# Optimization experiments

Hardware: AMD Instinct MI355X
Metric: run time of the kernel (lower is better)

## Reference

```python
import jax, jax.numpy as jnp
import numpy as np

NUM_HEADS = 12
SEG_HEADS = 6  # first 6 heads -> full attention; rest -> 4-way strided
HEAD_DIM = 64


def setup_inputs() -> dict:
    key = jax.random.key(0)
    ks = jax.random.split(key, 7)
    B, S, H = 2, 4096, 768
    sc = 0.02
    return {
        "hidden_states": jax.random.normal(ks[0], (B, S, H), jnp.float32),
        "Wq": jax.random.normal(ks[1], (H, H), jnp.float32) * sc,
        "bq": jax.random.normal(ks[2], (H,), jnp.float32) * sc,
        "Wk": jax.random.normal(ks[3], (H, H), jnp.float32) * sc,
        "bk": jax.random.normal(ks[4], (H,), jnp.float32) * sc,
        "Wv": jax.random.normal(ks[5], (H, H), jnp.float32) * sc,
        "bv": jax.random.normal(ks[6], (H,), jnp.float32) * sc,
    }


def _heads(x, B, S):
    # [B,S,H] -> [B,nH,S,D]
    return x.reshape(B, S, NUM_HEADS, HEAD_DIM).transpose(0, 2, 1, 3)


def reference(hidden_states, Wq, bq, Wk, bk, Wv, bv):
    B, S, H = hidden_states.shape
    scale = 1.0 / jnp.sqrt(jnp.float32(HEAD_DIM))

    q = _heads(hidden_states @ Wq.T + bq, B, S)
    k = _heads(hidden_states @ Wk.T + bk, B, S)
    v = _heads(hidden_states @ Wv.T + bv, B, S)

    # ---- full attention on first SEG_HEADS heads ----
    qf, kf, vf = q[:, :SEG_HEADS], k[:, :SEG_HEADS], v[:, :SEG_HEADS]
    scores = jnp.einsum('bhqd,bhkd->bhqk', qf, kf) * scale
    z_full = jnp.einsum('bhqk,bhkd->bhqd', jax.nn.softmax(scores, axis=-1), vf)

    # ---- 4-way strided attention on remaining heads ----
    # x[:,:,i::4,:] == reshape(B,h,S//4,4,D)[..., i, :]; batch the 4 groups.
    S4 = S // 4
    def strided(x):
        # [B,h,S,D] -> [B,h,4,S//4,D], group g holds positions g::4
        return x[:, SEG_HEADS:].reshape(B, NUM_HEADS - SEG_HEADS, S4, 4, HEAD_DIM).transpose(0, 1, 3, 2, 4)
    qa, ka, va = strided(q), strided(k), strided(v)
    s_ax = jnp.einsum('bhgqd,bhgkd->bhgqk', qa, ka) * scale
    z_ax = jnp.einsum('bhgqk,bhgkd->bhgqd', jax.nn.softmax(s_ax, axis=-1), va)
    # re-interleave: torch.stack(dim=3).view -> position s*4+g from (g,s)
    z_axis = z_ax.transpose(0, 1, 3, 2, 4).reshape(B, NUM_HEADS - SEG_HEADS, S, HEAD_DIM)

    ctx = jnp.concatenate([z_full, z_axis], axis=1)           # [B,nH,S,D]
    ctx = ctx.transpose(0, 2, 1, 3).reshape(B, S, NUM_HEADS * HEAD_DIM)
    return ctx
```

## Files before the change

### kernel.cpp

```cpp
#include <hip/hip_runtime.h>
#include <stdint.h>
#include <math.h>

#define BB 2
#define SS 4096
#define NHEADS 12
#define DHEAD 64

#define N_HS (8192*768)
#define N_W  (768*768)

typedef __bf16 bf16x8 __attribute__((ext_vector_type(8)));
typedef float  f32x4  __attribute__((ext_vector_type(4)));
typedef float  f32x16 __attribute__((ext_vector_type(16)));

__device__ __forceinline__ unsigned short f2bf(float x) {
  union { float f; uint32_t u; } v; v.f = x;
  uint32_t r = v.u + 0x7fffu + ((v.u >> 16) & 1u);
  return (unsigned short)(r >> 16);
}

__device__ __forceinline__ unsigned int pkbf(float a, float b) {
  union { __bf16 h[2]; unsigned int u; } t;
  t.h[0] = (__bf16)a; t.h[1] = (__bf16)b; return t.u;
}

__global__ __launch_bounds__(256) void convert_kernel(
    const float* __restrict__ hs, const float* __restrict__ wq,
    const float* __restrict__ wk, const float* __restrict__ wv,
    unsigned short* __restrict__ hs_bf, unsigned short* __restrict__ w_bf)
{
  int i = blockIdx.x * 256 + threadIdx.x;
  const int total4 = (N_HS + 3 * N_W) / 4;
  if (i >= total4) return;
  int e = i * 4;
  const float* src; int rel; unsigned short* dst; int dofs;
  if (e < N_HS) { src = hs; rel = e; dst = hs_bf; dofs = e; }
  else {
    int r = e - N_HS; dst = w_bf; dofs = r;
    if      (r < N_W)     { src = wq; rel = r; }
    else if (r < 2 * N_W) { src = wk; rel = r - N_W; }
    else                  { src = wv; rel = r - 2 * N_W; }
  }
  float4 v = *(const float4*)(src + rel);
  union { unsigned short s[4]; uint2 u; } o;
  o.s[0] = f2bf(v.x); o.s[1] = f2bf(v.y); o.s[2] = f2bf(v.z); o.s[3] = f2bf(v.w);
  *(uint2*)(dst + dofs) = o.u;
}

__global__ __launch_bounds__(256) void qkv_gemm(
    const unsigned short* __restrict__ hs,
    const unsigned short* __restrict__ w_all,
    const float* __restrict__ bq, const float* __restrict__ bk, const float* __restrict__ bv,
    unsigned short* __restrict__ qh,
    unsigned short* __restrict__ kh,
    unsigned short* __restrict__ vt)
{
  __shared__ __align__(16) unsigned short At[128 * 72];
  __shared__ __align__(16) unsigned short Bt[128 * 72];

  const int tid   = threadIdx.x;
  const int which = blockIdx.z;
  const int mbase = blockIdx.x * 128;
  const int nb    = blockIdx.y * 128;
  const unsigned short* w = w_all + (size_t)which * (768 * 768);
  const int lane = tid & 63, wid = tid >> 6;
  const int ln = lane & 15, qd = lane >> 4;
  const int wm = wid >> 1, wn = wid & 1;

  f32x4 acc[4][4];
#pragma unroll
  for (int i = 0; i < 4; i++)
#pragma unroll
    for (int j = 0; j < 4; j++) acc[i][j] = (f32x4){0.f, 0.f, 0.f, 0.f};

  for (int kb = 0; kb < 12; ++kb) {
    const int kbase = kb * 64;
    __syncthreads();
#pragma unroll
    for (int c = 0; c < 4; ++c) {
      int chn = c * 256 + tid;
      int row = chn >> 3, col8 = (chn & 7) * 8;
      *(uint4*)(&At[row * 72 + col8]) =
          *(const uint4*)(hs + (size_t)(mbase + row) * 768 + kbase + col8);
      *(uint4*)(&Bt[row * 72 + col8]) =
          *(const uint4*)(w + (size_t)(nb + row) * 768 + kbase + col8);
    }
    __syncthreads();
#pragma unroll
    for (int ks = 0; ks < 2; ++ks) {
      bf16x8 af[4], bfr[4];
#pragma unroll
      for (int t = 0; t < 4; t++) {
        af[t]  = *(const bf16x8*)(&At[(wm * 64 + t * 16 + ln) * 72 + qd * 8 + ks * 32]);
        bfr[t] = *(const bf16x8*)(&Bt[(wn * 64 + t * 16 + ln) * 72 + qd * 8 + ks * 32]);
      }
#pragma unroll
      for (int i = 0; i < 4; i++)
#pragma unroll
        for (int j = 0; j < 4; j++)
          acc[i][j] = __builtin_amdgcn_mfma_f32_16x16x32_bf16(af[i], bfr[j], acc[i][j], 0, 0, 0);
    }
  }

  const float* bias = (which == 0) ? bq : (which == 1) ? bk : bv;
  const float postscale = (which == 0) ? 0.18033688011112042f : 1.0f;
  if (which < 2) {
    unsigned short* dst = (which == 0) ? qh : kh;
#pragma unroll
    for (int j = 0; j < 4; j++) {
      int n = nb + wn * 64 + j * 16 + ln;
      float bb = bias[n];
      int hh = n >> 6, d = n & 63;
#pragma unroll
      for (int i = 0; i < 4; i++) {
#pragma unroll
        for (int r = 0; r < 4; r++) {
          int m = mbase + wm * 64 + i * 16 + qd * 4 + r;
          int b = m >> 12, s = m & 4095;
          dst[((size_t)(b * 12 + hh) * 4096 + s) * 64 + d] = f2bf((acc[i][j][r] + bb) * postscale);
        }
      }
    }
  } else {
#pragma unroll
    for (int j = 0; j < 4; j++) {
      int n = nb + wn * 64 + j * 16 + ln;
      float bb = bias[n];
      int hh = n >> 6, d = n & 63;
#pragma unroll
      for (int i = 0; i < 4; i++) {
        int m0 = mbase + wm * 64 + i * 16 + qd * 4;
        int b = m0 >> 12, s0 = m0 & 4095;
        size_t rowb = ((size_t)(b * 12 + hh) * 64 + d) * 4096;
        if (hh < 6) {
          union { unsigned short s[4]; uint2 u; } o4;
#pragma unroll
          for (int r = 0; r < 4; r++) o4.s[r] = f2bf(acc[i][j][r] + bb);
          *(uint2*)(&vt[rowb + s0]) = o4.u;
        } else {
          int i0 = s0 >> 2;
#pragma unroll
          for (int r = 0; r < 4; r++)
            vt[rowb + r * 1024 + i0] = f2bf(acc[i][j][r] + bb);
        }
      }
    }
  }
}

__device__ __forceinline__ void make_frags(const unsigned int* P, int hi,
                                           bf16x8* fa, bf16x8* fb) {
  unsigned int s0 = hi ? P[0] : P[2];
  unsigned int s1 = hi ? P[1] : P[3];
  unsigned int r0 = (unsigned int)__shfl_xor((int)s0, 32, 64);
  unsigned int r1 = (unsigned int)__shfl_xor((int)s1, 32, 64);
  unsigned int t0 = hi ? P[4] : P[6];
  unsigned int t1 = hi ? P[5] : P[7];
  unsigned int u0 = (unsigned int)__shfl_xor((int)t0, 32, 64);
  unsigned int u1 = (unsigned int)__shfl_xor((int)t1, 32, 64);
  union { unsigned int u[4]; bf16x8 v; } A, B;
  A.u[0] = hi ? r0 : P[0];
  A.u[1] = hi ? r1 : P[1];
  A.u[2] = hi ? P[2] : r0;
  A.u[3] = hi ? P[3] : r1;
  B.u[0] = hi ? u0 : P[4];
  B.u[1] = hi ? u1 : P[5];
  B.u[2] = hi ? P[6] : u0;
  B.u[3] = hi ? P[7] : u1;
  *fa = A.v; *fb = B.v;
}

__global__ __launch_bounds__(256) void attn_kernel(
    const unsigned short* __restrict__ qh,
    const unsigned short* __restrict__ kh,
    const unsigned short* __restrict__ vt,
    float* __restrict__ out,
    float* __restrict__ PO, float* __restrict__ PL)
{
  __shared__ __align__(16) unsigned short Kt[2 * 64 * 72];
  __shared__ __align__(16) unsigned short Vt[2 * 64 * 72];

  const int bid = blockIdx.x;
  int b, h, g, qt, nkt, kt0, strided, half, bh;
  if (bid < 768) {
    qt = bid & 31; half = (bid >> 5) & 1; bh = bid >> 6; b = bh / 6; h = bh % 6;
    g = 0; strided = 0; nkt = 32; kt0 = half * 32;
  } else {
    int r2 = bid - 768;
    qt = r2 & 7; r2 >>= 3; g = r2 & 3; r2 >>= 2; b = r2 / 6; h = 6 + r2 % 6;
    strided = 1; nkt = 16; kt0 = 0; half = 0; bh = 0;
  }
  const size_t headoff = (size_t)(b * 12 + h) * 4096 * 64;
  const unsigned short* qp = qh + headoff;
  const unsigned short* kp = kh + headoff;
  const unsigned short* vp = vt + headoff;

  const int tid = threadIdx.x;
  const int lane = tid & 63, w = tid >> 6;
  const int l32 = lane & 31, hi = lane >> 5;
  const int hi8 = hi * 8;

  const int qrow = qt * 128 + w * 32 + l32;
  const int sQ = strided ? (qrow * 4 + g) : qrow;
  bf16x8 qf[4];
#pragma unroll
  for (int c = 0; c < 4; ++c)
    qf[c] = *(const bf16x8*)(qp + (size_t)sQ * 64 + c * 16 + hi8);

  const int srow0 = tid >> 3,        scol0 = (tid & 7) * 8;
  const int srow1 = (tid + 256) >> 3, scol1 = ((tid + 256) & 7) * 8;
  const int s0g = kt0 * 64 + srow0, s1g = kt0 * 64 + srow1;
  const unsigned short* kptr0 = kp + (size_t)(strided ? (s0g * 4 + g) : s0g) * 64 + scol0;
  const unsigned short* kptr1 = kp + (size_t)(strided ? (s1g * 4 + g) : s1g) * 64 + scol1;
  const int vb0 = strided ? g * 1024 : 0;
  const unsigned short* vptr0 = vp + (size_t)srow0 * 4096 + vb0 + kt0 * 64 + scol0;
  const unsigned short* vptr1 = vp + (size_t)srow1 * 4096 + vb0 + kt0 * 64 + scol1;
  const int kstep = (strided ? 256 : 64) * 64;
  const int lofs0 = srow0 * 72 + scol0, lofs1 = srow1 * 72 + scol1;

  uint4 rk0 = *(const uint4*)kptr0, rk1 = *(const uint4*)kptr1;
  uint4 rv0 = *(const uint4*)vptr0, rv1 = *(const uint4*)vptr1;
  kptr0 += kstep; kptr1 += kstep; vptr0 += 64; vptr1 += 64;
  *(uint4*)(&Kt[lofs0]) = rk0; *(uint4*)(&Kt[lofs1]) = rk1;
  *(uint4*)(&Vt[lofs0]) = rv0; *(uint4*)(&Vt[lofs1]) = rv1;
  __syncthreads();

  f32x16 o0, o1;
#pragma unroll
  for (int i = 0; i < 16; i++) { o0[i] = 0.f; o1[i] = 0.f; }
  float lsum = 0.f;

  for (int kt = 0; kt < nkt; ++kt) {
    const int cur = (kt & 1) * 4608, nxt = 4608 - cur;
    const bool pf = (kt + 1 < nkt);
    if (pf) {
      rk0 = *(const uint4*)kptr0; rk1 = *(const uint4*)kptr1;
      rv0 = *(const uint4*)vptr0; rv1 = *(const uint4*)vptr1;
      kptr0 += kstep; kptr1 += kstep; vptr0 += 64; vptr1 += 64;
    }

    f32x16 sc0, sc1;
#pragma unroll
    for (int i = 0; i < 16; i++) { sc0[i] = 0.f; sc1[i] = 0.f; }
#pragma unroll
    for (int c = 0; c < 4; ++c) {
      bf16x8 k0 = *(const bf16x8*)(&Kt[cur + l32 * 72 + c * 16 + hi8]);
      sc0 = __builtin_amdgcn_mfma_f32_32x32x16_bf16(k0, qf[c], sc0, 0, 0, 0);
      bf16x8 k1 = *(const bf16x8*)(&Kt[cur + (32 + l32) * 72 + c * 16 + hi8]);
      sc1 = __builtin_amdgcn_mfma_f32_32x32x16_bf16(k1, qf[c], sc1, 0, 0, 0);
    }

    unsigned int P0[8], P1[8];
    float ls = 0.f;
#pragma unroll
    for (int u = 0; u < 8; ++u) {
      float a = exp2f(sc0[2 * u]);
      float c = exp2f(sc0[2 * u + 1]);
      ls += a + c;
      P0[u] = pkbf(a, c);
    }
#pragma unroll
    for (int u = 0; u < 8; ++u) {
      float a = exp2f(sc1[2 * u]);
      float c = exp2f(sc1[2 * u + 1]);
      ls += a + c;
      P1[u] = pkbf(a, c);
    }
    lsum += ls;

    bf16x8 pfr[4];
    make_frags(P0, hi, &pfr[0], &pfr[1]);
    make_frags(P1, hi, &pfr[2], &pfr[3]);

#pragma unroll
    for (int c = 0; c < 4; ++c) {
      bf16x8 v0 = *(const bf16x8*)(&Vt[cur + l32 * 72 + c * 16 + hi8]);
      o0 = __builtin_amdgcn_mfma_f32_32x32x16_bf16(v0, pfr[c], o0, 0, 0, 0);
      bf16x8 v1 = *(const bf16x8*)(&Vt[cur + (32 + l32) * 72 + c * 16 + hi8]);
      o1 = __builtin_amdgcn_mfma_f32_32x32x16_bf16(v1, pfr[c], o1, 0, 0, 0);
    }

    if (pf) {
      *(uint4*)(&Kt[nxt + lofs0]) = rk0; *(uint4*)(&Kt[nxt + lofs1]) = rk1;
      *(uint4*)(&Vt[nxt + lofs0]) = rv0; *(uint4*)(&Vt[nxt + lofs1]) = rv1;
    }
    __syncthreads();
  }

  float ltot = lsum + __shfl_xor(lsum, 32, 64);
  if (!strided) {
    size_t base = ((size_t)(bh * 2 + half) * 4096 + sQ) * 64;
#pragma unroll
    for (int mt = 0; mt < 2; ++mt) {
#pragma unroll
      for (int a = 0; a < 4; ++a) {
        float4 vv;
        vv.x = mt ? o1[4 * a + 0] : o0[4 * a + 0];
        vv.y = mt ? o1[4 * a + 1] : o0[4 * a + 1];
        vv.z = mt ? o1[4 * a + 2] : o0[4 * a + 2];
        vv.w = mt ? o1[4 * a + 3] : o0[4 * a + 3];
        *(float4*)(&PO[base + mt * 32 + a * 8 + hi * 4]) = vv;
      }
    }
    if (hi == 0) PL[(bh * 2 + half) * 4096 + sQ] = ltot;
  } else {
    float inv = 1.0f / ltot;
    size_t base = ((size_t)b * 4096 + sQ) * 768 + h * 64;
#pragma unroll
    for (int mt = 0; mt < 2; ++mt) {
#pragma unroll
      for (int a = 0; a < 4; ++a) {
        float4 vv;
        vv.x = (mt ? o1[4 * a + 0] : o0[4 * a + 0]) * inv;
        vv.y = (mt ? o1[4 * a + 1] : o0[4 * a + 1]) * inv;
        vv.z = (mt ? o1[4 * a + 2] : o0[4 * a + 2]) * inv;
        vv.w = (mt ? o1[4 * a + 3] : o0[4 * a + 3]) * inv;
        *(float4*)(&out[base + mt * 32 + a * 8 + hi * 4]) = vv;
      }
    }
  }
}

__global__ __launch_bounds__(256) void merge_kernel(
    const float* __restrict__ PO, const float* __restrict__ PL,
    float* __restrict__ out)
{
  int i = blockIdx.x * 256 + threadIdx.x;
  int c4 = i & 15;
  int qrow = (i >> 4) & 4095;
  int bh = i >> 16;
  size_t p0 = (((size_t)bh * 2 + 0) * 4096 + qrow) * 64 + c4 * 4;
  size_t p1 = (((size_t)bh * 2 + 1) * 4096 + qrow) * 64 + c4 * 4;
  float4 a = *(const float4*)(&PO[p0]);
  float4 c = *(const float4*)(&PO[p1]);
  float l = PL[(bh * 2 + 0) * 4096 + qrow] + PL[(bh * 2 + 1) * 4096 + qrow];
  float inv = 1.0f / l;
  float4 o;
  o.x = (a.x + c.x) * inv; o.y = (a.y + c.y) * inv;
  o.z = (a.z + c.z) * inv; o.w = (a.w + c.w) * inv;
  int b = bh / 6, h = bh % 6;
  *(float4*)(&out[((size_t)b * 4096 + qrow) * 768 + h * 64 + c4 * 4]) = o;
}

extern "C" void kernel_launch(void* const* d_in, const int* in_sizes, int n_in,
                              void* d_out, int out_size, void* d_ws, size_t ws_size,
                              hipStream_t stream) {
  const float* hs = (const float*)d_in[0];
  const float* Wq = (const float*)d_in[1];
  const float* bq = (const float*)d_in[2];
  const float* Wk = (const float*)d_in[3];
  const float* bk = (const float*)d_in[4];
  const float* Wv = (const float*)d_in[5];
  const float* bv = (const float*)d_in[6];
  float* out = (float*)d_out;

  unsigned short* q_bf  = (unsigned short*)d_ws;
  unsigned short* k_bf  = q_bf + (size_t)BB * NHEADS * SS * DHEAD;
  unsigned short* vt_bf = k_bf + (size_t)BB * NHEADS * SS * DHEAD;
  unsigned short* hs_bf = vt_bf + (size_t)BB * NHEADS * SS * DHEAD;
  unsigned short* w_bf  = hs_bf + (size_t)N_HS;
  float* PO = (float*)hs_bf;
  float* PL = PO + (size_t)12 * 2 * 4096 * 64;

  const int total4 = (N_HS + 3 * N_W) / 4;
  convert_kernel<<<(total4 + 255) / 256, 256, 0, stream>>>(hs, Wq, Wk, Wv, hs_bf, w_bf);

  dim3 ggrid(64, 6, 3);
  qkv_gemm<<<ggrid, 256, 0, stream>>>(hs_bf, w_bf, bq, bk, bv, q_bf, k_bf, vt_bf);

  attn_kernel<<<1152, 256, 0, stream>>>(q_bf, k_bf, vt_bf, out, PO, PL);

  merge_kernel<<<3072, 256, 0, stream>>>(PO, PL, out);
}
```

Baseline: 264.0 us.

## Use direct global-to-LDS loads with XOR swizzle, fast exp2, MFMA row sums

The QKV GEMM now stages tiles with global_load_lds straight into an XOR-swizzled, unpadded LDS layout, so data no longer passes through registers and padding is not needed to avoid bank conflicts. The attention kernel uses the hardware exp2 builtin and truncates to bf16 with a byte permute instead of round-to-nearest. The softmax denominator is now computed by an extra MFMA of a ones matrix against the P fragments, replacing scalar accumulation and a shuffle. This trades some extra MFMA work and slightly less precise P values for fewer VALU instructions.

Result: faster. 241.8 us (-8.4%).

```diff
diff --git a/kernel.cpp b/kernel.cpp
--- a/kernel.cpp
+++ b/kernel.cpp
@@ -20,9 +20,26 @@
   return (unsigned short)(r >> 16);
 }
 
-__device__ __forceinline__ unsigned int pkbf(float a, float b) {
-  union { __bf16 h[2]; unsigned int u; } t;
-  t.h[0] = (__bf16)a; t.h[1] = (__bf16)b; return t.u;
+__device__ __forceinline__ float fexp2(float x) {
+#if __has_builtin(__builtin_amdgcn_exp2f)
+  return __builtin_amdgcn_exp2f(x);
+#else
+  return exp2f(x);
+#endif
+}
+
+__device__ __forceinline__ unsigned int pk_trunc(float lo, float hi) {
+#if __has_builtin(__builtin_amdgcn_perm)
+  return __builtin_amdgcn_perm(__float_as_uint(hi), __float_as_uint(lo), 0x07060302u);
+#else
+  return (__float_as_uint(hi) & 0xffff0000u) | (__float_as_uint(lo) >> 16);
+#endif
+}
+
+__device__ __forceinline__ void gld16(const unsigned short* g, unsigned short* l) {
+  __builtin_amdgcn_global_load_lds(
+      (const __attribute__((address_space(1))) unsigned int*)g,
+      (__attribute__((address_space(3))) unsigned int*)l, 16, 0, 0);
 }
 
 __global__ __launch_bounds__(256) void convert_kernel(
@@ -56,8 +73,8 @@
     unsigned short* __restrict__ kh,
     unsigned short* __restrict__ vt)
 {
-  __shared__ __align__(16) unsigned short At[128 * 72];
-  __shared__ __align__(16) unsigned short Bt[128 * 72];
+  __shared__ __align__(16) unsigned short At[128 * 64];
+  __shared__ __align__(16) unsigned short Bt[128 * 64];
 
   const int tid   = threadIdx.x;
   const int which = blockIdx.z;
@@ -68,6 +85,9 @@
   const int ln = lane & 15, qd = lane >> 4;
   const int wm = wid >> 1, wn = wid & 1;
 
+  const int srow = lane >> 3;
+  const int sslot = (lane & 7) ^ srow;
+
   f32x4 acc[4][4];
 #pragma unroll
   for (int i = 0; i < 4; i++)
@@ -78,13 +98,11 @@
     const int kbase = kb * 64;
     __syncthreads();
 #pragma unroll
-    for (int c = 0; c < 4; ++c) {
-      int chn = c * 256 + tid;
-      int row = chn >> 3, col8 = (chn & 7) * 8;
-      *(uint4*)(&At[row * 72 + col8]) =
-          *(const uint4*)(hs + (size_t)(mbase + row) * 768 + kbase + col8);
-      *(uint4*)(&Bt[row * 72 + col8]) =
-          *(const uint4*)(w + (size_t)(nb + row) * 768 + kbase + col8);
+    for (int j = 0; j < 4; ++j) {
+      int c = wid * 4 + j;
+      int row = c * 8 + srow;
+      gld16(hs + (size_t)(mbase + row) * 768 + kbase + sslot * 8, &At[c * 512]);
+      gld16(w  + (size_t)(nb    + row) * 768 + kbase + sslot * 8, &Bt[c * 512]);
     }
     __syncthreads();
 #pragma unroll
@@ -92,8 +110,11 @@
       bf16x8 af[4], bfr[4];
 #pragma unroll
       for (int t = 0; t < 4; t++) {
-        af[t]  = *(const bf16x8*)(&At[(wm * 64 + t * 16 + ln) * 72 + qd * 8 + ks * 32]);
-        bfr[t] = *(const bf16x8*)(&Bt[(wn * 64 + t * 16 + ln) * 72 + qd * 8 + ks * 32]);
+        int ra = wm * 64 + t * 16 + ln;
+        int rb = wn * 64 + t * 16 + ln;
+        int slot = (qd + 4 * ks);
+        af[t]  = *(const bf16x8*)(&At[ra * 64 + ((slot ^ (ra & 7)) * 8)]);
+        bfr[t] = *(const bf16x8*)(&Bt[rb * 64 + ((slot ^ (rb & 7)) * 8)]);
       }
 #pragma unroll
       for (int i = 0; i < 4; i++)
@@ -208,6 +229,11 @@
   for (int c = 0; c < 4; ++c)
     qf[c] = *(const bf16x8*)(qp + (size_t)sQ * 64 + c * 16 + hi8);
 
+  union { unsigned int u[4]; bf16x8 v; } ones_;
+#pragma unroll
+  for (int i = 0; i < 4; i++) ones_.u[i] = 0x3f803f80u;
+  const bf16x8 onesf = ones_.v;
+
   const int srow0 = tid >> 3,        scol0 = (tid & 7) * 8;
   const int srow1 = (tid + 256) >> 3, scol1 = ((tid + 256) & 7) * 8;
   const int s0g = kt0 * 64 + srow0, s1g = kt0 * 64 + srow1;
@@ -226,10 +252,9 @@
   *(uint4*)(&Vt[lofs0]) = rv0; *(uint4*)(&Vt[lofs1]) = rv1;
   __syncthreads();
 
-  f32x16 o0, o1;
-#pragma unroll
-  for (int i = 0; i < 16; i++) { o0[i] = 0.f; o1[i] = 0.f; }
-  float lsum = 0.f;
+  f32x16 o0, o1, lacc;
+#pragma unroll
+  for (int i = 0; i < 16; i++) { o0[i] = 0.f; o1[i] = 0.f; lacc[i] = 0.f; }
 
   for (int kt = 0; kt < nkt; ++kt) {
     const int cur = (kt & 1) * 4608, nxt = 4608 - cur;
@@ -252,22 +277,18 @@
     }
 
     unsigned int P0[8], P1[8];
-    float ls = 0.f;
 #pragma unroll
     for (int u = 0; u < 8; ++u) {
-      float a = exp2f(sc0[2 * u]);
-      float c = exp2f(sc0[2 * u + 1]);
-      ls += a + c;
-      P0[u] = pkbf(a, c);
+      float a = fexp2(sc0[2 * u]);
+      float c = fexp2(sc0[2 * u + 1]);
+      P0[u] = pk_trunc(a, c);
     }
 #pragma unroll
     for (int u = 0; u < 8; ++u) {
-      float a = exp2f(sc1[2 * u]);
-      float c = exp2f(sc1[2 * u + 1]);
-      ls += a + c;
-      P1[u] = pkbf(a, c);
-    }
-    lsum += ls;
+      float a = fexp2(sc1[2 * u]);
+      float c = fexp2(sc1[2 * u + 1]);
+      P1[u] = pk_trunc(a, c);
+    }
 
     bf16x8 pfr[4];
     make_frags(P0, hi, &pfr[0], &pfr[1]);
@@ -279,6 +300,7 @@
       o0 = __builtin_amdgcn_mfma_f32_32x32x16_bf16(v0, pfr[c], o0, 0, 0, 0);
       bf16x8 v1 = *(const bf16x8*)(&Vt[cur + (32 + l32) * 72 + c * 16 + hi8]);
       o1 = __builtin_amdgcn_mfma_f32_32x32x16_bf16(v1, pfr[c], o1, 0, 0, 0);
+      lacc = __builtin_amdgcn_mfma_f32_32x32x16_bf16(onesf, pfr[c], lacc, 0, 0, 0);
     }
 
     if (pf) {
@@ -288,7 +310,7 @@
     __syncthreads();
   }
 
-  float ltot = lsum + __shfl_xor(lsum, 32, 64);
+  const float ltot = lacc[0];
   if (!strided) {
     size_t base = ((size_t)(bh * 2 + half) * 4096 + sQ) * 64;
 #pragma unroll
```
